# Kernel tuning notes

Measured on AMD Instinct MI355X. Metric: run time of the kernel, lower is better.

Reference implementation:

```python
import jax, jax.numpy as jnp
import numpy as np

N_NODES = 100000
N_EDGES = 1250000
D_FEAT = 64


def setup_inputs() -> dict:
    key = jax.random.key(0)
    kx, ke = jax.random.split(key)
    x = jax.random.normal(kx, (N_NODES, D_FEAT), dtype=jnp.float32)
    edge_index = jax.random.randint(ke, (2, N_EDGES), 0, N_NODES, dtype=jnp.int64)
    return {"x": x, "edge_index": edge_index}


def reference(x, edge_index):
    # propagate: scatter_nested gathers x[idxj] grouped by destination idxi
    # (a ragged per-node neighbor set); the module's sum_nested reduces each
    # group. Expressed densely and jit-ably as gather + segment-sum.
    idxi = edge_index[0, :]  # destination nodes
    idxj = edge_index[1, :]  # source nodes
    messages = x[idxj]  # [E, D] edge-level gather (memory-bound)
    out = jax.ops.segment_sum(messages, idxi, num_segments=N_NODES)  # [N, D]
    return out
```

## Files before the change

kernel.cpp:

```cpp
#include <hip/hip_runtime.h>

#define N_NODES 100000
#define N_EDGES 1250000
#define D_FEAT  64

#define SB_SHIFT 9
#define SB_NODES 512
#define NSB      ((N_NODES + SB_NODES - 1) / SB_NODES)
#define SBCAP    7168
#define OVF_CAP  32768

#define K1_BLOCKS  1024
#define K1_THREADS 512
#define K1_STRIDE  (K1_BLOCKS * K1_THREADS)
#define K1_ITERS   ((N_EDGES + K1_STRIDE - 1) / K1_STRIDE)

#define NPB   64
#define NBLK  ((N_NODES + NPB - 1) / NPB)
#define KCAP  1280

__global__ __launch_bounds__(K1_THREADS) void k1_bin_kernel(
        const int* __restrict__ idxi, const int* __restrict__ idxj,
        int* __restrict__ gcursor, int* __restrict__ ovfcnt,
        int* __restrict__ ovf, int* __restrict__ binbuf) {
    __shared__ int hist[NSB];
    __shared__ int gbase[NSB];
    __shared__ int cur[NSB];
    int t = threadIdx.x;
    if (t < NSB) hist[t] = 0;
    __syncthreads();

    int dd[K1_ITERS], ss[K1_ITERS];
    int e0 = blockIdx.x * K1_THREADS + t;
#pragma unroll
    for (int j = 0; j < K1_ITERS; ++j) {
        int e = e0 + j * K1_STRIDE;
        if (e < N_EDGES) {
            dd[j] = idxi[e];
            ss[j] = idxj[e];
            atomicAdd(&hist[dd[j] >> SB_SHIFT], 1);
        } else {
            dd[j] = -1;
        }
    }
    __syncthreads();

    if (t < NSB) {
        int h = hist[t];
        gbase[t] = h ? atomicAdd(&gcursor[t], h) : 0;
        cur[t] = 0;
    }
    __syncthreads();

#pragma unroll
    for (int j = 0; j < K1_ITERS; ++j) {
        if (dd[j] >= 0) {
            int b = dd[j] >> SB_SHIFT;
            int pos = gbase[b] + atomicAdd(&cur[b], 1);
            if (pos < SBCAP) {
                binbuf[b * SBCAP + pos] = ((dd[j] & (SB_NODES - 1)) << 17) | ss[j];
            } else {
                int op = atomicAdd(ovfcnt, 1);
                if (op < OVF_CAP) { ovf[2 * op] = dd[j]; ovf[2 * op + 1] = ss[j]; }
            }
        }
    }
}

__global__ __launch_bounds__(256) void k23_gather_kernel(
        const float* __restrict__ x, const int* __restrict__ gcursor,
        const int* __restrict__ binbuf, int* __restrict__ ovfcnt,
        int* __restrict__ ovf, float* __restrict__ out) {
    __shared__ int cnt[NPB];
    __shared__ int excl[NPB];
    __shared__ int cur[NPB];
    __shared__ int klist[KCAP];
    __shared__ int srt[KCAP];
    __shared__ int nk;

    int bid = blockIdx.x;
    int nwg = NBLK;
    int xcd = bid & 7;
    int lid = bid >> 3;
    int q = nwg >> 3, r = nwg & 7;
    int blk = (xcd < r ? xcd * (q + 1) : r * (q + 1) + (xcd - r) * q) + lid;

    int t = threadIdx.x;
    int lane = t & 63;
    if (t < NPB) cnt[t] = 0;
    if (t == 0) nk = 0;
    __syncthreads();

    int sb  = blk >> 3;
    int my3 = blk & 7;
    int n = gcursor[sb];
    if (n > SBCAP) n = SBCAP;
    const int* buf = binbuf + (size_t)sb * SBCAP;

    for (int i0 = 0; i0 < n; i0 += 256) {
        int i = i0 + t;
        int p = (i < n) ? buf[i] : -1;
        bool keep = (p >= 0) && ((p >> 23) == my3);
        unsigned long long m = __ballot(keep);
        int tot = __popcll(m);
        int base;
        if (lane == 0) base = atomicAdd(&nk, tot);
        base = __shfl(base, 0, 64);
        if (keep) {
            int pos = base + __popcll(m & ((1ull << lane) - 1));
            if (pos < KCAP) {
                klist[pos] = p;
                atomicAdd(&cnt[(p >> 17) & (NPB - 1)], 1);
            } else {
                int op = atomicAdd(ovfcnt, 1);
                if (op < OVF_CAP) {
                    ovf[2 * op]     = blk * NPB + ((p >> 17) & (NPB - 1));
                    ovf[2 * op + 1] = p & 0x1FFFF;
                }
            }
        }
    }
    __syncthreads();

    if (t < NPB) {
        int v = cnt[t];
        int vinc = v;
#pragma unroll
        for (int off = 1; off < NPB; off <<= 1) {
            int u = __shfl_up(vinc, off, 64);
            if (lane >= off) vinc += u;
        }
        excl[t] = vinc - v;
        cur[t] = 0;
    }
    __syncthreads();

    int kn = nk;
    if (kn > KCAP) kn = KCAP;
    for (int i = t; i < kn; i += 256) {
        int p = klist[i];
        int dl = (p >> 17) & (NPB - 1);
        int pos = excl[dl] + atomicAdd(&cur[dl], 1);
        srt[pos] = p & 0x1FFFF;
    }
    __syncthreads();

    int wave = t >> 6;
    int sub  = lane >> 4;
    int c4   = lane & 15;
    const float4* xp = (const float4*)x;
    for (int nd = 0; nd < 4; ++nd) {
        int dl = wave * 16 + sub * 4 + nd;
        int node = blk * NPB + dl;
        int k = excl[dl];
        int end = k + cnt[dl];
        float4 acc = make_float4(0.f, 0.f, 0.f, 0.f);
        for (; k + 4 <= end; k += 4) {
            int s0 = srt[k], s1 = srt[k + 1], s2 = srt[k + 2], s3 = srt[k + 3];
            float4 v0 = xp[s0 * 16 + c4];
            float4 v1 = xp[s1 * 16 + c4];
            float4 v2 = xp[s2 * 16 + c4];
            float4 v3 = xp[s3 * 16 + c4];
            acc.x += (v0.x + v1.x) + (v2.x + v3.x);
            acc.y += (v0.y + v1.y) + (v2.y + v3.y);
            acc.z += (v0.z + v1.z) + (v2.z + v3.z);
            acc.w += (v0.w + v1.w) + (v2.w + v3.w);
        }
        for (; k < end; ++k) {
            float4 v0 = xp[srt[k] * 16 + c4];
            acc.x += v0.x; acc.y += v0.y; acc.z += v0.z; acc.w += v0.w;
        }
        if (node < N_NODES) {
            ((float4*)out)[(size_t)node * 16 + c4] = acc;
        }
    }
}

__global__ __launch_bounds__(256) void ovf_fixup_kernel(
        const float* __restrict__ x, const int* __restrict__ ovfcnt,
        const int* __restrict__ ovf, float* __restrict__ out) {
    int n = *ovfcnt;
    if (n > OVF_CAP) n = OVF_CAP;
    long long total = (long long)n * 16;
    long long stride = (long long)gridDim.x * blockDim.x;
    for (long long t = blockIdx.x * blockDim.x + threadIdx.x; t < total; t += stride) {
        int e  = (int)(t >> 4);
        int fo = ((int)t & 15) << 2;
        int d = ovf[2 * e];
        int s = ovf[2 * e + 1];
        const float4 v = *(const float4*)(x + (size_t)s * D_FEAT + fo);
        float* o = out + (size_t)d * D_FEAT + fo;
        atomicAdd(o + 0, v.x);
        atomicAdd(o + 1, v.y);
        atomicAdd(o + 2, v.z);
        atomicAdd(o + 3, v.w);
    }
}


__global__ __launch_bounds__(256) void zero_f4_kernel(float* __restrict__ out, int n4) {
    int i = blockIdx.x * blockDim.x + threadIdx.x;
    if (i < n4) ((float4*)out)[i] = make_float4(0.f, 0.f, 0.f, 0.f);
}

__global__ __launch_bounds__(256) void scatter_add_kernel(const float* __restrict__ x,
                                                          const int* __restrict__ idxi,
                                                          const int* __restrict__ idxj,
                                                          float* __restrict__ out) {
    int t = blockIdx.x * blockDim.x + threadIdx.x;
    int e = t >> 4;
    if (e >= N_EDGES) return;
    int fo = (t & 15) << 2;
    int dst = idxi[e];
    int src = idxj[e];
    const float4 v = *(const float4*)(x + (size_t)src * D_FEAT + fo);
    float* o = out + (size_t)dst * D_FEAT + fo;
    atomicAdd(o + 0, v.x);
    atomicAdd(o + 1, v.y);
    atomicAdd(o + 2, v.z);
    atomicAdd(o + 3, v.w);
}

extern "C" void kernel_launch(void* const* d_in, const int* in_sizes, int n_in,
                              void* d_out, int out_size, void* d_ws, size_t ws_size,
                              hipStream_t stream) {
    const float* x  = (const float*)d_in[0];
    const int*   ei = (const int*)d_in[1];
    const int*   idxi = ei;
    const int*   idxj = ei + N_EDGES;
    float* out = (float*)d_out;

    {
        size_t need = (256 + 16 + 2 * (size_t)OVF_CAP +
                       (size_t)NSB * SBCAP) * sizeof(int);
        if (ws_size >= need) {
            int* gcursor = (int*)d_ws;
            int* ovfcnt  = gcursor + 256;
            int* ovf     = ovfcnt + 16;
            int* binbuf  = ovf + 2 * OVF_CAP;

            hipMemsetAsync(gcursor, 0, (256 + 16) * sizeof(int), stream);
            k1_bin_kernel<<<K1_BLOCKS, K1_THREADS, 0, stream>>>(idxi, idxj, gcursor,
                                                                ovfcnt, ovf, binbuf);
            k23_gather_kernel<<<NBLK, 256, 0, stream>>>(x, gcursor, binbuf,
                                                        ovfcnt, ovf, out);
            ovf_fixup_kernel<<<16, 256, 0, stream>>>(x, ovfcnt, ovf, out);
            return;
        }
    }

    int n4 = (N_NODES * D_FEAT) / 4;
    zero_f4_kernel<<<(n4 + 255) / 256, 256, 0, stream>>>(out, n4);
    long long total_threads = (long long)N_EDGES * 16;
    scatter_add_kernel<<<(int)((total_threads + 255) / 256), 256, 0, stream>>>(x, idxi, idxj, out);
}
```

Before: 160.9 us.

## Stage binned edges in LDS for coalesced writes; accumulate gathers via LDS atomics

The binning kernel now gives each block a contiguous chunk of 2048 edges. It sorts the chunk by super-bin in shared memory using a local prefix scan, so writes to the global bin buffer come out as contiguous runs instead of scattered stores. The gather kernel drops its per-node counting sort and instead accumulates x rows straight into a 64x64 float LDS tile with shared-memory atomics, one row per wave, four edges in flight at a time. This removes two sort passes and their barriers, in exchange for LDS atomic contention and a larger LDS footprint per block, which may lower occupancy.

Measured after the change: 582.9 us. 3.62x slower.

```diff
diff --git a/kernel.cpp b/kernel.cpp
--- a/kernel.cpp
+++ b/kernel.cpp
@@ -10,10 +10,10 @@
 #define SBCAP    7168
 #define OVF_CAP  32768
 
-#define K1_BLOCKS  1024
-#define K1_THREADS 512
-#define K1_STRIDE  (K1_BLOCKS * K1_THREADS)
-#define K1_ITERS   ((N_EDGES + K1_STRIDE - 1) / K1_STRIDE)
+#define K1_THREADS 256
+#define EPB        2048
+#define EPT        (EPB / K1_THREADS)
+#define K1B        ((N_EDGES + EPB - 1) / EPB)
 
 #define NPB   64
 #define NBLK  ((N_NODES + NPB - 1) / NPB)
@@ -24,24 +24,50 @@
         int* __restrict__ gcursor, int* __restrict__ ovfcnt,
         int* __restrict__ ovf, int* __restrict__ binbuf) {
     __shared__ int hist[NSB];
+    __shared__ int runstart[NSB];
     __shared__ int gbase[NSB];
     __shared__ int cur[NSB];
+    __shared__ int staged[EPB];
+    __shared__ unsigned char sbin[EPB];
     int t = threadIdx.x;
     if (t < NSB) hist[t] = 0;
     __syncthreads();
 
-    int dd[K1_ITERS], ss[K1_ITERS];
-    int e0 = blockIdx.x * K1_THREADS + t;
-#pragma unroll
-    for (int j = 0; j < K1_ITERS; ++j) {
-        int e = e0 + j * K1_STRIDE;
-        if (e < N_EDGES) {
-            dd[j] = idxi[e];
-            ss[j] = idxj[e];
-            atomicAdd(&hist[dd[j] >> SB_SHIFT], 1);
+    int base = blockIdx.x * EPB;
+    int n = N_EDGES - base; if (n > EPB) n = EPB;
+    int d[EPT], s[EPT];
+#pragma unroll
+    for (int j = 0; j < EPT; ++j) {
+        int i = t + j * K1_THREADS;
+        if (i < n) {
+            d[j] = idxi[base + i];
+            s[j] = idxj[base + i];
+            atomicAdd(&hist[d[j] >> SB_SHIFT], 1);
         } else {
-            dd[j] = -1;
-        }
+            d[j] = -1;
+        }
+    }
+    __syncthreads();
+
+    if (t < 64) {
+        int b0 = 4 * t;
+        int h0 = (b0     < NSB) ? hist[b0]     : 0;
+        int h1 = (b0 + 1 < NSB) ? hist[b0 + 1] : 0;
+        int h2 = (b0 + 2 < NSB) ? hist[b0 + 2] : 0;
+        int h3 = (b0 + 3 < NSB) ? hist[b0 + 3] : 0;
+        int s01 = h0 + h1;
+        int sum = s01 + h2 + h3;
+        int inc = sum;
+#pragma unroll
+        for (int off = 1; off < 64; off <<= 1) {
+            int u = __shfl_up(inc, off, 64);
+            if (t >= off) inc += u;
+        }
+        int ex = inc - sum;
+        if (b0     < NSB) runstart[b0]     = ex;
+        if (b0 + 1 < NSB) runstart[b0 + 1] = ex + h0;
+        if (b0 + 2 < NSB) runstart[b0 + 2] = ex + s01;
+        if (b0 + 3 < NSB) runstart[b0 + 3] = ex + s01 + h2;
     }
     __syncthreads();
 
@@ -53,16 +79,25 @@
     __syncthreads();
 
 #pragma unroll
-    for (int j = 0; j < K1_ITERS; ++j) {
-        if (dd[j] >= 0) {
-            int b = dd[j] >> SB_SHIFT;
-            int pos = gbase[b] + atomicAdd(&cur[b], 1);
-            if (pos < SBCAP) {
-                binbuf[b * SBCAP + pos] = ((dd[j] & (SB_NODES - 1)) << 17) | ss[j];
-            } else {
-                int op = atomicAdd(ovfcnt, 1);
-                if (op < OVF_CAP) { ovf[2 * op] = dd[j]; ovf[2 * op + 1] = ss[j]; }
-            }
+    for (int j = 0; j < EPT; ++j) {
+        if (d[j] >= 0) {
+            int b = d[j] >> SB_SHIFT;
+            int idx = runstart[b] + atomicAdd(&cur[b], 1);
+            staged[idx] = ((d[j] & (SB_NODES - 1)) << 17) | s[j];
+            sbin[idx] = (unsigned char)b;
+        }
+    }
+    __syncthreads();
+
+    for (int i = t; i < n; i += K1_THREADS) {
+        int b = sbin[i];
+        int p = staged[i];
+        int tgt = gbase[b] + (i - runstart[b]);
+        if (tgt < SBCAP) {
+            binbuf[b * SBCAP + tgt] = p;
+        } else {
+            int op = atomicAdd(ovfcnt, 1);
+            if (op < OVF_CAP) { ovf[2 * op] = (b << SB_SHIFT) | (p >> 17); ovf[2 * op + 1] = p & 0x1FFFF; }
         }
     }
 }
@@ -71,23 +106,21 @@
         const float* __restrict__ x, const int* __restrict__ gcursor,
         const int* __restrict__ binbuf, int* __restrict__ ovfcnt,
         int* __restrict__ ovf, float* __restrict__ out) {
-    __shared__ int cnt[NPB];
-    __shared__ int excl[NPB];
-    __shared__ int cur[NPB];
+    __shared__ __align__(16) float acc[NPB * D_FEAT];
     __shared__ int klist[KCAP];
-    __shared__ int srt[KCAP];
     __shared__ int nk;
 
     int bid = blockIdx.x;
-    int nwg = NBLK;
-    int xcd = bid & 7;
-    int lid = bid >> 3;
-    int q = nwg >> 3, r = nwg & 7;
+    int q = NBLK >> 3, r = NBLK & 7;
+    int xcd = bid & 7, lid = bid >> 3;
     int blk = (xcd < r ? xcd * (q + 1) : r * (q + 1) + (xcd - r) * q) + lid;
 
     int t = threadIdx.x;
     int lane = t & 63;
-    if (t < NPB) cnt[t] = 0;
+    int w = t >> 6;
+#pragma unroll
+    for (int j = 0; j < (NPB * D_FEAT / 4) / 256; ++j)
+        ((float4*)acc)[t + j * 256] = make_float4(0.f, 0.f, 0.f, 0.f);
     if (t == 0) nk = 0;
     __syncthreads();
 
@@ -100,21 +133,20 @@
     for (int i0 = 0; i0 < n; i0 += 256) {
         int i = i0 + t;
         int p = (i < n) ? buf[i] : -1;
-        bool keep = (p >= 0) && ((p >> 23) == my3);
+        bool keep = (p >= 0) && (((p >> 23) & 7) == my3);
         unsigned long long m = __ballot(keep);
         int tot = __popcll(m);
-        int base;
-        if (lane == 0) base = atomicAdd(&nk, tot);
-        base = __shfl(base, 0, 64);
+        int bpos;
+        if (lane == 0) bpos = atomicAdd(&nk, tot);
+        bpos = __shfl(bpos, 0, 64);
         if (keep) {
-            int pos = base + __popcll(m & ((1ull << lane) - 1));
+            int pos = bpos + __popcll(m & ((1ull << lane) - 1));
             if (pos < KCAP) {
                 klist[pos] = p;
-                atomicAdd(&cnt[(p >> 17) & (NPB - 1)], 1);
             } else {
                 int op = atomicAdd(ovfcnt, 1);
                 if (op < OVF_CAP) {
-                    ovf[2 * op]     = blk * NPB + ((p >> 17) & (NPB - 1));
+                    ovf[2 * op]     = (sb << SB_SHIFT) | (p >> 17);
                     ovf[2 * op + 1] = p & 0x1FFFF;
                 }
             }
@@ -122,57 +154,33 @@
     }
     __syncthreads();
 
-    if (t < NPB) {
-        int v = cnt[t];
-        int vinc = v;
-#pragma unroll
-        for (int off = 1; off < NPB; off <<= 1) {
-            int u = __shfl_up(vinc, off, 64);
-            if (lane >= off) vinc += u;
-        }
-        excl[t] = vinc - v;
-        cur[t] = 0;
-    }
-    __syncthreads();
-
     int kn = nk;
     if (kn > KCAP) kn = KCAP;
-    for (int i = t; i < kn; i += 256) {
-        int p = klist[i];
-        int dl = (p >> 17) & (NPB - 1);
-        int pos = excl[dl] + atomicAdd(&cur[dl], 1);
-        srt[pos] = p & 0x1FFFF;
-    }
-    __syncthreads();
-
-    int wave = t >> 6;
-    int sub  = lane >> 4;
-    int c4   = lane & 15;
-    const float4* xp = (const float4*)x;
-    for (int nd = 0; nd < 4; ++nd) {
-        int dl = wave * 16 + sub * 4 + nd;
-        int node = blk * NPB + dl;
-        int k = excl[dl];
-        int end = k + cnt[dl];
-        float4 acc = make_float4(0.f, 0.f, 0.f, 0.f);
-        for (; k + 4 <= end; k += 4) {
-            int s0 = srt[k], s1 = srt[k + 1], s2 = srt[k + 2], s3 = srt[k + 3];
-            float4 v0 = xp[s0 * 16 + c4];
-            float4 v1 = xp[s1 * 16 + c4];
-            float4 v2 = xp[s2 * 16 + c4];
-            float4 v3 = xp[s3 * 16 + c4];
-            acc.x += (v0.x + v1.x) + (v2.x + v3.x);
-            acc.y += (v0.y + v1.y) + (v2.y + v3.y);
-            acc.z += (v0.z + v1.z) + (v2.z + v3.z);
-            acc.w += (v0.w + v1.w) + (v2.w + v3.w);
-        }
-        for (; k < end; ++k) {
-            float4 v0 = xp[srt[k] * 16 + c4];
-            acc.x += v0.x; acc.y += v0.y; acc.z += v0.z; acc.w += v0.w;
-        }
-        if (node < N_NODES) {
-            ((float4*)out)[(size_t)node * 16 + c4] = acc;
-        }
+    for (int k0 = w * 4; k0 < kn; k0 += 16) {
+        int pk0 = klist[k0];
+        int pk1 = (k0 + 1 < kn) ? klist[k0 + 1] : -1;
+        int pk2 = (k0 + 2 < kn) ? klist[k0 + 2] : -1;
+        int pk3 = (k0 + 3 < kn) ? klist[k0 + 3] : -1;
+        float v0 = x[(size_t)(pk0 & 0x1FFFF) * D_FEAT + lane];
+        float v1 = (pk1 >= 0) ? x[(size_t)(pk1 & 0x1FFFF) * D_FEAT + lane] : 0.f;
+        float v2 = (pk2 >= 0) ? x[(size_t)(pk2 & 0x1FFFF) * D_FEAT + lane] : 0.f;
+        float v3 = (pk3 >= 0) ? x[(size_t)(pk3 & 0x1FFFF) * D_FEAT + lane] : 0.f;
+        atomicAdd(&acc[((pk0 >> 17) & 63) * D_FEAT + lane], v0);
+        if (pk1 >= 0) atomicAdd(&acc[((pk1 >> 17) & 63) * D_FEAT + lane], v1);
+        if (pk2 >= 0) atomicAdd(&acc[((pk2 >> 17) & 63) * D_FEAT + lane], v2);
+        if (pk3 >= 0) atomicAdd(&acc[((pk3 >> 17) & 63) * D_FEAT + lane], v3);
+    }
+    __syncthreads();
+
+    int base_node = blk * NPB;
+    const float4* a4 = (const float4*)acc;
+#pragma unroll
+    for (int j = 0; j < 4; ++j) {
+        int qq = t + j * 256;
+        int dl = qq >> 4, c4 = qq & 15;
+        int node = base_node + dl;
+        if (node < N_NODES)
+            ((float4*)out)[(size_t)node * 16 + c4] = a4[qq];
     }
 }
 
@@ -240,8 +248,8 @@
             int* binbuf  = ovf + 2 * OVF_CAP;
 
             hipMemsetAsync(gcursor, 0, (256 + 16) * sizeof(int), stream);
-            k1_bin_kernel<<<K1_BLOCKS, K1_THREADS, 0, stream>>>(idxi, idxj, gcursor,
-                                                                ovfcnt, ovf, binbuf);
+            k1_bin_kernel<<<K1B, K1_THREADS, 0, stream>>>(idxi, idxj, gcursor,
+                                                          ovfcnt, ovf, binbuf);
             k23_gather_kernel<<<NBLK, 256, 0, stream>>>(x, gcursor, binbuf,
                                                         ovfcnt, ovf, out);
             ovf_fixup_kernel<<<16, 256, 0, stream>>>(x, ovfcnt, ovf, out);
```
